# Kernel tuning notes

Hardware: AMD Instinct MI355X
Metric: run time of the kernel (lower is better)

The kernel has to match this reference:

```python
import jax, jax.numpy as jnp
import numpy as np

B, I, H, OH = 16384, 256, 256, 64
N_STEPS = 8  # fixed-step dopri5 (adaptive step control replaced by fixed grid for jit)


def setup_inputs() -> dict:
    key = jax.random.key(0)
    ks = jax.random.split(key, 12)
    sH = 1.0 / np.sqrt(H)
    sOH = 1.0 / np.sqrt(OH)
    u = lambda k, shape, s: jax.random.uniform(k, shape, jnp.float32, -s, s)
    return {
        "input": jax.random.normal(ks[0], (B, I), jnp.float32),
        "h_prev": jax.random.normal(ks[1], (B, H), jnp.float32),
        "c_prev": jax.random.normal(ks[2], (B, H), jnp.float32),
        "timespans": jax.random.uniform(ks[3], (B,), jnp.float32, 0.05, 1.0),
        # LSTMCell params (PyTorch layout: gates stacked as [i, f, g, o])
        "W_ih": u(ks[4], (4 * H, I), sH),
        "W_hh": u(ks[5], (4 * H, H), sH),
        "b_ih": u(ks[6], (4 * H,), sH),
        "b_hh": u(ks[7], (4 * H,), sH),
        # ode_func: Linear(H, OH) -> Tanh -> Linear(OH, H)
        "W1": u(ks[8], (OH, H), sH),
        "b1": u(ks[9], (OH,), sH),
        "W2": u(ks[10], (H, OH), sOH),
        "b2": u(ks[11], (H,), sOH),
    }


def reference(input, h_prev, c_prev, timespans, W_ih, W_hh, b_ih, b_hh, W1, b1, W2, b2):
    # --- LSTMCell ---
    gates = input @ W_ih.T + b_ih + h_prev @ W_hh.T + b_hh  # (B, 4H)
    gi, gf, gg, go = jnp.split(gates, 4, axis=-1)
    i = jax.nn.sigmoid(gi)
    f = jax.nn.sigmoid(gf)
    g = jnp.tanh(gg)
    o = jax.nn.sigmoid(go)
    c = f * c_prev + i * g
    h = o * jnp.tanh(c)

    # --- Neural ODE: dy/dt = MLP(y), autonomous, Dormand-Prince RK45 ---
    def ode_f(y):
        return jnp.tanh(y @ W1.T + b1) @ W2.T + b2

    dt = (timespans / N_STEPS)[:, None]  # (B, 1) per-sample step size

    def dopri5_step(y, _):
        k1 = ode_f(y)
        k2 = ode_f(y + dt * (1.0 / 5.0 * k1))
        k3 = ode_f(y + dt * (3.0 / 40.0 * k1 + 9.0 / 40.0 * k2))
        k4 = ode_f(y + dt * (44.0 / 45.0 * k1 - 56.0 / 15.0 * k2 + 32.0 / 9.0 * k3))
        k5 = ode_f(y + dt * (19372.0 / 6561.0 * k1 - 25360.0 / 2187.0 * k2
                             + 64448.0 / 6561.0 * k3 - 212.0 / 729.0 * k4))
        k6 = ode_f(y + dt * (9017.0 / 3168.0 * k1 - 355.0 / 33.0 * k2
                             + 46732.0 / 5247.0 * k3 + 49.0 / 176.0 * k4
                             - 5103.0 / 18656.0 * k5))
        y_next = y + dt * (35.0 / 384.0 * k1 + 500.0 / 1113.0 * k3 + 125.0 / 192.0 * k4
                           - 2187.0 / 6784.0 * k5 + 11.0 / 84.0 * k6)
        return y_next, None

    h_ode, _ = jax.lax.scan(dopri5_step, h, None, length=N_STEPS)
    return h_ode, c
```

## Files before the change

kernel.cpp:

```cpp
#include <hip/hip_runtime.h>
#include <hip/hip_bf16.h>


#define B_N 16384
#define H_N 256

typedef __attribute__((ext_vector_type(8))) short short8;
typedef __attribute__((ext_vector_type(4))) unsigned short u16x4;
typedef __attribute__((ext_vector_type(4))) float f32x4;

__device__ __forceinline__ unsigned short f2bf_s(float x) {
  __hip_bfloat16 h = __float2bfloat16(x);
  return *reinterpret_cast<unsigned short*>(&h);
}

__device__ __forceinline__ short8 pack8f(const float* p) {
  const f32x4 a = *(const f32x4*)p;
  const f32x4 b = *(const f32x4*)(p + 4);
  short8 r;
  r[0] = (short)f2bf_s(a[0]); r[1] = (short)f2bf_s(a[1]);
  r[2] = (short)f2bf_s(a[2]); r[3] = (short)f2bf_s(a[3]);
  r[4] = (short)f2bf_s(b[0]); r[5] = (short)f2bf_s(b[1]);
  r[6] = (short)f2bf_s(b[2]); r[7] = (short)f2bf_s(b[3]);
  return r;
}

__device__ __forceinline__ u16x4 pack4(f32x4 v) {
  u16x4 r;
  r[0] = f2bf_s(v[0]); r[1] = f2bf_s(v[1]);
  r[2] = f2bf_s(v[2]); r[3] = f2bf_s(v[3]);
  return r;
}

__device__ __forceinline__ float fast_sigmoid(float x) {
  return __builtin_amdgcn_rcpf(1.f + __expf(-x));
}
__device__ __forceinline__ float fast_tanh(float x) {
  x = fminf(15.f, fmaxf(-15.f, x));
  float e = __expf(2.f * x);
  return 1.f - 2.f * __builtin_amdgcn_rcpf(e + 1.f);
}

__device__ __forceinline__ void gl_lds16(const void* g, void* l) {
  __builtin_amdgcn_global_load_lds(
      (const __attribute__((address_space(1))) void*)g,
      (__attribute__((address_space(3))) void*)l, 16, 0, 0);
}

__global__ __launch_bounds__(256) void prep_kernel(
    const float* __restrict__ Wih, const float* __restrict__ Whh,
    const float* __restrict__ W1, const float* __restrict__ W2,
    const float* __restrict__ b2,
    unsigned short* __restrict__ wsB, unsigned short* __restrict__ wcB,
    float* __restrict__ uF) {
  const int bx = blockIdx.x;
  if (bx < 256) {
    int idx = bx * 256 + threadIdx.x;
    int n = idx >> 6, c = idx & 63, k = c * 8;
    const float* src = (k < 256) ? (Wih + (size_t)n * 256 + k)
                                 : (Whh + (size_t)n * 256 + (k - 256));
    *(short8*)(wsB + (size_t)n * 512 + k) = pack8f(src);
  } else if (bx < 272) {
    int idx = (bx - 256) * 256 + threadIdx.x;
    int f = idx >> 6, o = idx & 63;
    float a0 = 0.f, a1 = 0.f, a2 = 0.f, a3 = 0.f;
    for (int h = 0; h < 256; h += 4) {
      a0 = fmaf(W1[f * 256 + h],     W2[h * 64 + o],        a0);
      a1 = fmaf(W1[f * 256 + h + 1], W2[(h + 1) * 64 + o],  a1);
      a2 = fmaf(W1[f * 256 + h + 2], W2[(h + 2) * 64 + o],  a2);
      a3 = fmaf(W1[f * 256 + h + 3], W2[(h + 3) * 64 + o],  a3);
    }
    wcB[f * 64 + o] = f2bf_s((a0 + a1) + (a2 + a3));
  } else {
    int f = threadIdx.x;
    if (f < 64) {
      float a0 = 0.f, a1 = 0.f, a2 = 0.f, a3 = 0.f;
      for (int h = 0; h < 256; h += 4) {
        a0 = fmaf(W1[f * 256 + h],     b2[h],     a0);
        a1 = fmaf(W1[f * 256 + h + 1], b2[h + 1], a1);
        a2 = fmaf(W1[f * 256 + h + 2], b2[h + 2], a2);
        a3 = fmaf(W1[f * 256 + h + 3], b2[h + 3], a3);
      }
      uF[f] = (a0 + a1) + (a2 + a3);
    }
  }
}

__global__ __launch_bounds__(512, 4) void lstm_kernel(
    const float* __restrict__ x, const float* __restrict__ hp,
    const float* __restrict__ cp, const unsigned short* __restrict__ wsB,
    const float* __restrict__ bih, const float* __restrict__ bhh,
    float* __restrict__ out) {
  __shared__ __align__(16) float As2[2][128 * 32];
  __shared__ __align__(16) unsigned short Bs2[2][256 * 32];

  const int tid = threadIdx.x;
  const int lane = tid & 63;
  const int wv = tid >> 6;
  const int rg = wv >> 1;
  const int cg = wv & 1;
  const int s = lane & 15, q = lane >> 4;
  const int mb = blockIdx.x * 128;
  const int hb = blockIdx.y * 64;

  f32x4 acc[2][8];
#pragma unroll
  for (int mt = 0; mt < 2; ++mt)
#pragma unroll
    for (int tn = 0; tn < 8; ++tn) acc[mt][tn] = (f32x4){0.f, 0.f, 0.f, 0.f};

  const int c16a = wv * 2;
  const int rowA0 = c16a * 8 + (lane >> 3);
  const int gcA = (lane & 7) ^ (rowA0 & 7);
  const int rowB0 = c16a * 16 + (lane >> 2);
  const int rowB1 = rowB0 + 16;
  const int gcB0 = (lane & 3) ^ ((rowB0 >> 1) & 3);
  const int gcB1 = (lane & 3) ^ ((rowB1 >> 1) & 3);
  const int grB0 = (rowB0 >> 6) * 256 + hb + (rowB0 & 63);
  const int grB1 = (rowB1 >> 6) * 256 + hb + (rowB1 & 63);

  auto STAGE = [&](int buf, int kt) {
    const float* srcA = (kt < 8) ? x : hp;
    const int kl = (kt * 32) & 255;
    gl_lds16(srcA + (size_t)(mb + rowA0) * 256 + kl + gcA * 4,
             (char*)As2[buf] + c16a * 1024);
    gl_lds16(srcA + (size_t)(mb + rowA0 + 8) * 256 + kl + gcA * 4,
             (char*)As2[buf] + (c16a + 1) * 1024);
    gl_lds16(wsB + (size_t)grB0 * 512 + kt * 32 + gcB0 * 8,
             (char*)Bs2[buf] + c16a * 1024);
    gl_lds16(wsB + (size_t)grB1 * 512 + kt * 32 + gcB1 * 8,
             (char*)Bs2[buf] + (c16a + 1) * 1024);
  };

  STAGE(0, 0);
  __syncthreads();

  for (int kt = 0; kt < 16; ++kt) {
    const int buf = kt & 1;
    if (kt < 15) STAGE(buf ^ 1, kt + 1);

    short8 af[2];
#pragma unroll
    for (int mt = 0; mt < 2; ++mt) {
      const int ar = rg * 32 + mt * 16 + s;
      const char* ap = (const char*)As2[buf] + ar * 128;
      float tmp[8];
      *(f32x4*)tmp = *(const f32x4*)(ap + (((q * 2) ^ (ar & 7)) << 4));
      *(f32x4*)(tmp + 4) = *(const f32x4*)(ap + (((q * 2 + 1) ^ (ar & 7)) << 4));
      af[mt] = pack8f(tmp);
    }
    const char* bp = (const char*)Bs2[buf];
#pragma unroll
    for (int tn = 0; tn < 8; ++tn) {
      const int t = (tn >> 1) * 64 + cg * 32 + (tn & 1) * 16 + s;
      short8 bfr = *(const short8*)(bp + t * 64 + ((q ^ ((t >> 1) & 3)) << 4));
      acc[0][tn] = __builtin_amdgcn_mfma_f32_16x16x32_bf16(af[0], bfr, acc[0][tn], 0, 0, 0);
      acc[1][tn] = __builtin_amdgcn_mfma_f32_16x16x32_bf16(af[1], bfr, acc[1][tn], 0, 0, 0);
    }
    __syncthreads();
  }

#pragma unroll
  for (int mt = 0; mt < 2; ++mt)
#pragma unroll
    for (int ntl = 0; ntl < 2; ++ntl)
#pragma unroll
      for (int r = 0; r < 4; ++r) {
        int sample = mb + rg * 32 + mt * 16 + q * 4 + r;
        int h = hb + cg * 32 + ntl * 16 + s;
        float gi = acc[mt][0 + ntl][r] + bih[h] + bhh[h];
        float gf = acc[mt][2 + ntl][r] + bih[256 + h] + bhh[256 + h];
        float gg = acc[mt][4 + ntl][r] + bih[512 + h] + bhh[512 + h];
        float go = acc[mt][6 + ntl][r] + bih[768 + h] + bhh[768 + h];
        float iv = fast_sigmoid(gi), fv = fast_sigmoid(gf);
        float gv = fast_tanh(gg), ov = fast_sigmoid(go);
        float c = fv * cp[(size_t)sample * 256 + h] + iv * gv;
        float hv = ov * fast_tanh(c);
        out[(size_t)B_N * H_N + (size_t)sample * 256 + h] = c;
        out[(size_t)sample * 256 + h] = hv;
      }
}

__global__ __launch_bounds__(256, 4) void ode_kernel(
    float* __restrict__ out, const float* __restrict__ ts,
    const float* __restrict__ W1, const unsigned short* __restrict__ wcB,
    const float* __restrict__ uF, const float* __restrict__ W2,
    const float* __restrict__ b1, const float* __restrict__ b2) {
  __shared__ __align__(16) unsigned short zcA[16 * 64];
  __shared__ __align__(16) unsigned short zcB2[16 * 64];
  char* zA = (char*)zcA;
  char* zB = (char*)zcB2;

  const int tid = threadIdx.x;
  const int lane = tid & 63, wv = tid >> 6;
  const int s = lane & 15, q = lane >> 4;
  const int bb = blockIdx.x * 16;
  const int sx7 = s & 7;

  short8 wcf[2];
#pragma unroll
  for (int kt = 0; kt < 2; ++kt)
    wcf[kt] = *(const short8*)(wcB + (size_t)(wv * 16 + s) * 64 + kt * 32 + q * 8);

  const f32x4 b1v = *(const f32x4*)(b1 + wv * 16 + q * 4);
  const f32x4 u4 = *(const f32x4*)(uF + wv * 16 + q * 4);
  const float dt = ts[bb + s] * 0.125f;

  f32x4 yreg[4];
#pragma unroll
  for (int i = 0; i < 4; ++i)
    yreg[i] = *(const f32x4*)(out + (size_t)(bb + s) * 256 + wv * 64 + i * 16 + q * 4);

  f32x4 G = (f32x4){0.f, 0.f, 0.f, 0.f};
#pragma unroll
  for (int kt = 0; kt < 8; ++kt) {
    short8 w1f = pack8f(W1 + (size_t)(wv * 16 + s) * 256 + kt * 32 + q * 8);
    short8 yf = pack8f(out + (size_t)(bb + s) * 256 + kt * 32 + q * 8);
    G = __builtin_amdgcn_mfma_f32_16x16x32_bf16(w1f, yf, G, 0, 0, 0);
  }

  const int zwoff = (((wv * 2 + (q >> 1)) ^ sx7) << 4) + (q & 1) * 8;
  const int rb = s * 128;

  auto stz = [&](char* buf, f32x4 v) { *(u16x4*)(buf + rb + zwoff) = pack4(v); };
  auto wcmm = [&](const char* buf) -> f32x4 {
    const char* rp = buf + rb;
    short8 zf0 = *(const short8*)(rp + ((q ^ sx7) << 4));
    short8 zf1 = *(const short8*)(rp + (((4 + q) ^ sx7) << 4));
    f32x4 a = (f32x4){0.f, 0.f, 0.f, 0.f};
    a = __builtin_amdgcn_mfma_f32_16x16x32_bf16(wcf[0], zf0, a, 0, 0, 0);
    a = __builtin_amdgcn_mfma_f32_16x16x32_bf16(wcf[1], zf1, a, 0, 0, 0);
    return a;
  };
  auto stage = [&](char* buf, f32x4 zc, float cj) -> f32x4 {
    stz(buf, zc);
    __syncthreads();
    f32x4 o = wcmm(buf);
    f32x4 zo;
#pragma unroll
    for (int r = 0; r < 4; ++r)
      zo[r] = fast_tanh(fmaf(dt, fmaf(cj, u4[r], o[r]), G[r]) + b1v[r]);
    return zo;
  };

  const float A31 = 3.f / 40.f, A32 = 9.f / 40.f;
  const float A41 = 44.f / 45.f, A42 = -56.f / 15.f, A43 = 32.f / 9.f;
  const float A51 = 19372.f / 6561.f, A52 = -25360.f / 2187.f,
              A53 = 64448.f / 6561.f, A54 = -212.f / 729.f;
  const float A61 = 9017.f / 3168.f, A62 = -355.f / 33.f, A63 = 46732.f / 5247.f,
              A64 = 49.f / 176.f, A65 = -5103.f / 18656.f;
  const float C1 = 35.f / 384.f, C3 = 500.f / 1113.f, C4 = 125.f / 192.f,
              C5 = -2187.f / 6784.f, C6 = 11.f / 84.f;

  f32x4 SC = (f32x4){0.f, 0.f, 0.f, 0.f};

  for (int st = 0; st < 8; ++st) {
    f32x4 z1;
#pragma unroll
    for (int r = 0; r < 4; ++r) z1[r] = fast_tanh(G[r] + b1v[r]);

    f32x4 z2 = stage(zA, 0.2f * z1, 0.2f);
    f32x4 z3 = stage(zB, A31 * z1 + A32 * z2, 0.3f);
    f32x4 z4 = stage(zA, A41 * z1 + A42 * z2 + A43 * z3, 0.8f);
    f32x4 z5 = stage(zB, A51 * z1 + A52 * z2 + A53 * z3 + A54 * z4, 8.f / 9.f);
    f32x4 z6 = stage(zA, A61 * z1 + A62 * z2 + A63 * z3 + A64 * z4 + A65 * z5, 1.0f);

    f32x4 zc = C1 * z1 + C3 * z3 + C4 * z4 + C5 * z5 + C6 * z6;
    stz(zB, zc);
    __syncthreads();
    f32x4 o6 = wcmm(zB);
    SC += zc;
#pragma unroll
    for (int r = 0; r < 4; ++r) G[r] = fmaf(dt, u4[r] + o6[r], G[r]);
  }

  stz(zA, SC);
  __syncthreads();
  {
    const char* rp = zA + rb;
    short8 zf0 = *(const short8*)(rp + ((q ^ sx7) << 4));
    short8 zf1 = *(const short8*)(rp + (((4 + q) ^ sx7) << 4));
#pragma unroll
    for (int i = 0; i < 4; ++i) {
      short8 w2f0 = pack8f(W2 + (size_t)(wv * 64 + i * 16 + s) * 64 + q * 8);
      short8 w2f1 = pack8f(W2 + (size_t)(wv * 64 + i * 16 + s) * 64 + 32 + q * 8);
      f32x4 a = (f32x4){0.f, 0.f, 0.f, 0.f};
      a = __builtin_amdgcn_mfma_f32_16x16x32_bf16(w2f0, zf0, a, 0, 0, 0);
      a = __builtin_amdgcn_mfma_f32_16x16x32_bf16(w2f1, zf1, a, 0, 0, 0);
      f32x4 b2v = *(const f32x4*)(b2 + wv * 64 + i * 16 + q * 4);
#pragma unroll
      for (int r = 0; r < 4; ++r)
        yreg[i][r] = fmaf(dt, fmaf(8.f, b2v[r], a[r]), yreg[i][r]);
    }
  }

#pragma unroll
  for (int i = 0; i < 4; ++i)
    *(f32x4*)(out + (size_t)(bb + s) * 256 + wv * 64 + i * 16 + q * 4) = yreg[i];
}

extern "C" void kernel_launch(void* const* d_in, const int* in_sizes, int n_in,
                              void* d_out, int out_size, void* d_ws, size_t ws_size,
                              hipStream_t stream) {
  const float* x   = (const float*)d_in[0];
  const float* hp  = (const float*)d_in[1];
  const float* cp  = (const float*)d_in[2];
  const float* ts  = (const float*)d_in[3];
  const float* Wih = (const float*)d_in[4];
  const float* Whh = (const float*)d_in[5];
  const float* bih = (const float*)d_in[6];
  const float* bhh = (const float*)d_in[7];
  const float* W1  = (const float*)d_in[8];
  const float* b1  = (const float*)d_in[9];
  const float* W2  = (const float*)d_in[10];
  const float* b2  = (const float*)d_in[11];
  float* out = (float*)d_out;

  unsigned short* wsB = (unsigned short*)d_ws;
  unsigned short* wcB = wsB + 1024 * 512;
  float* uF = (float*)((char*)d_ws + 1024 * 1024 + 8192);

  prep_kernel<<<273, 256, 0, stream>>>(Wih, Whh, W1, W2, b2, wsB, wcB, uF);
  lstm_kernel<<<dim3(128, 4), 512, 0, stream>>>(x, hp, cp, wsB, bih, bhh, out);
  ode_kernel<<<1024, 256, 0, stream>>>(out, ts, W1, wcB, uF, W2, b1, b2);
}
```

Measured before the change: 79.05 us.

## Run ODE solver with one wave per block to drop block barriers

Restructures the ODE kernel from four waves per 16-sample block to a single 64-lane wave. That wave computes all four 16-column tiles of the hidden projection, so the per-stage z exchange through LDS needs only a waitcnt instead of __syncthreads. W1 and W2 are pre-converted to bf16 in the prep kernel rather than packed per block. The tanh clamp is also removed. The single-wave blocks carry more registers per lane and give less latency hiding per block. Without the clamp, exp overflow to inf in tanh still gives ±1 through rcp, so it should stay safe.

```diff
diff --git a/kernel.cpp b/kernel.cpp
--- a/kernel.cpp
+++ b/kernel.cpp
@@ -36,7 +36,6 @@
   return __builtin_amdgcn_rcpf(1.f + __expf(-x));
 }
 __device__ __forceinline__ float fast_tanh(float x) {
-  x = fminf(15.f, fmaxf(-15.f, x));
   float e = __expf(2.f * x);
   return 1.f - 2.f * __builtin_amdgcn_rcpf(e + 1.f);
 }
@@ -52,7 +51,8 @@
     const float* __restrict__ W1, const float* __restrict__ W2,
     const float* __restrict__ b2,
     unsigned short* __restrict__ wsB, unsigned short* __restrict__ wcB,
-    float* __restrict__ uF) {
+    float* __restrict__ uF, unsigned short* __restrict__ w1B,
+    unsigned short* __restrict__ w2B) {
   const int bx = blockIdx.x;
   if (bx < 256) {
     int idx = bx * 256 + threadIdx.x;
@@ -71,7 +71,7 @@
       a3 = fmaf(W1[f * 256 + h + 3], W2[(h + 3) * 64 + o],  a3);
     }
     wcB[f * 64 + o] = f2bf_s((a0 + a1) + (a2 + a3));
-  } else {
+  } else if (bx == 272) {
     int f = threadIdx.x;
     if (f < 64) {
       float a0 = 0.f, a1 = 0.f, a2 = 0.f, a3 = 0.f;
@@ -83,6 +83,12 @@
       }
       uF[f] = (a0 + a1) + (a2 + a3);
     }
+  } else if (bx < 281) {
+    int idx = (bx - 273) * 256 + threadIdx.x;
+    *(short8*)(w1B + (size_t)idx * 8) = pack8f(W1 + (size_t)idx * 8);
+  } else {
+    int idx = (bx - 281) * 256 + threadIdx.x;
+    *(short8*)(w2B + (size_t)idx * 8) = pack8f(W2 + (size_t)idx * 8);
   }
 }
 
@@ -181,66 +187,74 @@
       }
 }
 
-__global__ __launch_bounds__(256, 4) void ode_kernel(
+__global__ __launch_bounds__(64) void ode_kernel(
     float* __restrict__ out, const float* __restrict__ ts,
-    const float* __restrict__ W1, const unsigned short* __restrict__ wcB,
-    const float* __restrict__ uF, const float* __restrict__ W2,
+    const unsigned short* __restrict__ wcB, const float* __restrict__ uF,
+    const unsigned short* __restrict__ w1B, const unsigned short* __restrict__ w2B,
     const float* __restrict__ b1, const float* __restrict__ b2) {
-  __shared__ __align__(16) unsigned short zcA[16 * 64];
-  __shared__ __align__(16) unsigned short zcB2[16 * 64];
-  char* zA = (char*)zcA;
-  char* zB = (char*)zcB2;
-
-  const int tid = threadIdx.x;
-  const int lane = tid & 63, wv = tid >> 6;
+  __shared__ __align__(16) unsigned short zbuf[16 * 80];
+  char* zb = (char*)zbuf;
+
+  const int lane = threadIdx.x;
   const int s = lane & 15, q = lane >> 4;
   const int bb = blockIdx.x * 16;
-  const int sx7 = s & 7;
-
-  short8 wcf[2];
-#pragma unroll
-  for (int kt = 0; kt < 2; ++kt)
-    wcf[kt] = *(const short8*)(wcB + (size_t)(wv * 16 + s) * 64 + kt * 32 + q * 8);
-
-  const f32x4 b1v = *(const f32x4*)(b1 + wv * 16 + q * 4);
-  const f32x4 u4 = *(const f32x4*)(uF + wv * 16 + q * 4);
+  const int wb = s * 160;
+
+  short8 wcf[4][2];
+#pragma unroll
+  for (int i = 0; i < 4; ++i)
+#pragma unroll
+    for (int kt = 0; kt < 2; ++kt)
+      wcf[i][kt] = *(const short8*)(wcB + (size_t)(i * 16 + s) * 64 + kt * 32 + q * 8);
+  f32x4 b1v[4], u4[4];
+#pragma unroll
+  for (int i = 0; i < 4; ++i) {
+    b1v[i] = *(const f32x4*)(b1 + i * 16 + q * 4);
+    u4[i] = *(const f32x4*)(uF + i * 16 + q * 4);
+  }
   const float dt = ts[bb + s] * 0.125f;
 
-  f32x4 yreg[4];
-#pragma unroll
-  for (int i = 0; i < 4; ++i)
-    yreg[i] = *(const f32x4*)(out + (size_t)(bb + s) * 256 + wv * 64 + i * 16 + q * 4);
-
-  f32x4 G = (f32x4){0.f, 0.f, 0.f, 0.f};
+  f32x4 G[4];
+#pragma unroll
+  for (int i = 0; i < 4; ++i) G[i] = (f32x4){0.f, 0.f, 0.f, 0.f};
 #pragma unroll
   for (int kt = 0; kt < 8; ++kt) {
-    short8 w1f = pack8f(W1 + (size_t)(wv * 16 + s) * 256 + kt * 32 + q * 8);
     short8 yf = pack8f(out + (size_t)(bb + s) * 256 + kt * 32 + q * 8);
-    G = __builtin_amdgcn_mfma_f32_16x16x32_bf16(w1f, yf, G, 0, 0, 0);
-  }
-
-  const int zwoff = (((wv * 2 + (q >> 1)) ^ sx7) << 4) + (q & 1) * 8;
-  const int rb = s * 128;
-
-  auto stz = [&](char* buf, f32x4 v) { *(u16x4*)(buf + rb + zwoff) = pack4(v); };
-  auto wcmm = [&](const char* buf) -> f32x4 {
-    const char* rp = buf + rb;
-    short8 zf0 = *(const short8*)(rp + ((q ^ sx7) << 4));
-    short8 zf1 = *(const short8*)(rp + (((4 + q) ^ sx7) << 4));
-    f32x4 a = (f32x4){0.f, 0.f, 0.f, 0.f};
-    a = __builtin_amdgcn_mfma_f32_16x16x32_bf16(wcf[0], zf0, a, 0, 0, 0);
-    a = __builtin_amdgcn_mfma_f32_16x16x32_bf16(wcf[1], zf1, a, 0, 0, 0);
-    return a;
+#pragma unroll
+    for (int i = 0; i < 4; ++i) {
+      short8 w1f = *(const short8*)(w1B + (size_t)(i * 16 + s) * 256 + kt * 32 + q * 8);
+      G[i] = __builtin_amdgcn_mfma_f32_16x16x32_bf16(w1f, yf, G[i], 0, 0, 0);
+    }
+  }
+
+  auto exch = [&](const f32x4 (&v)[4]) {
+#pragma unroll
+    for (int i = 0; i < 4; ++i)
+      *(u16x4*)(zb + wb + i * 32 + q * 8) = pack4(v[i]);
+    asm volatile("s_waitcnt lgkmcnt(0)" ::: "memory");
+    __builtin_amdgcn_sched_barrier(0);
   };
-  auto stage = [&](char* buf, f32x4 zc, float cj) -> f32x4 {
-    stz(buf, zc);
-    __syncthreads();
-    f32x4 o = wcmm(buf);
-    f32x4 zo;
-#pragma unroll
-    for (int r = 0; r < 4; ++r)
-      zo[r] = fast_tanh(fmaf(dt, fmaf(cj, u4[r], o[r]), G[r]) + b1v[r]);
-    return zo;
+  auto wcmm = [&](f32x4 (&o)[4]) {
+    short8 zf0 = *(const short8*)(zb + wb + q * 16);
+    short8 zf1 = *(const short8*)(zb + wb + 64 + q * 16);
+#pragma unroll
+    for (int i = 0; i < 4; ++i) {
+      f32x4 a = (f32x4){0.f, 0.f, 0.f, 0.f};
+      a = __builtin_amdgcn_mfma_f32_16x16x32_bf16(wcf[i][0], zf0, a, 0, 0, 0);
+      a = __builtin_amdgcn_mfma_f32_16x16x32_bf16(wcf[i][1], zf1, a, 0, 0, 0);
+      o[i] = a;
+    }
+  };
+  auto stage = [&](const f32x4 (&zc)[4], float cj, f32x4 (&zo)[4]) {
+    exch(zc);
+    f32x4 o[4];
+    wcmm(o);
+#pragma unroll
+    for (int i = 0; i < 4; ++i)
+#pragma unroll
+      for (int r = 0; r < 4; ++r)
+        zo[i][r] =
+            fast_tanh(fmaf(dt, fmaf(cj, u4[i][r], o[i][r]), G[i][r]) + b1v[i][r]);
   };
 
   const float A31 = 3.f / 40.f, A32 = 9.f / 40.f;
@@ -252,51 +266,80 @@
   const float C1 = 35.f / 384.f, C3 = 500.f / 1113.f, C4 = 125.f / 192.f,
               C5 = -2187.f / 6784.f, C6 = 11.f / 84.f;
 
-  f32x4 SC = (f32x4){0.f, 0.f, 0.f, 0.f};
+  f32x4 SC[4];
+#pragma unroll
+  for (int i = 0; i < 4; ++i) SC[i] = (f32x4){0.f, 0.f, 0.f, 0.f};
+  f32x4 z1[4], z2[4], z3[4], z4[4], z5[4], zc[4];
 
   for (int st = 0; st < 8; ++st) {
-    f32x4 z1;
-#pragma unroll
-    for (int r = 0; r < 4; ++r) z1[r] = fast_tanh(G[r] + b1v[r]);
-
-    f32x4 z2 = stage(zA, 0.2f * z1, 0.2f);
-    f32x4 z3 = stage(zB, A31 * z1 + A32 * z2, 0.3f);
-    f32x4 z4 = stage(zA, A41 * z1 + A42 * z2 + A43 * z3, 0.8f);
-    f32x4 z5 = stage(zB, A51 * z1 + A52 * z2 + A53 * z3 + A54 * z4, 8.f / 9.f);
-    f32x4 z6 = stage(zA, A61 * z1 + A62 * z2 + A63 * z3 + A64 * z4 + A65 * z5, 1.0f);
-
-    f32x4 zc = C1 * z1 + C3 * z3 + C4 * z4 + C5 * z5 + C6 * z6;
-    stz(zB, zc);
-    __syncthreads();
-    f32x4 o6 = wcmm(zB);
-    SC += zc;
-#pragma unroll
-    for (int r = 0; r < 4; ++r) G[r] = fmaf(dt, u4[r] + o6[r], G[r]);
-  }
-
-  stz(zA, SC);
-  __syncthreads();
+#pragma unroll
+    for (int i = 0; i < 4; ++i)
+#pragma unroll
+      for (int r = 0; r < 4; ++r) z1[i][r] = fast_tanh(G[i][r] + b1v[i][r]);
+
+#pragma unroll
+    for (int i = 0; i < 4; ++i) zc[i] = 0.2f * z1[i];
+    stage(zc, 0.2f, z2);
+#pragma unroll
+    for (int i = 0; i < 4; ++i) zc[i] = A31 * z1[i] + A32 * z2[i];
+    stage(zc, 0.3f, z3);
+#pragma unroll
+    for (int i = 0; i < 4; ++i) zc[i] = A41 * z1[i] + A42 * z2[i] + A43 * z3[i];
+    stage(zc, 0.8f, z4);
+#pragma unroll
+    for (int i = 0; i < 4; ++i)
+      zc[i] = A51 * z1[i] + A52 * z2[i] + A53 * z3[i] + A54 * z4[i];
+    stage(zc, 8.f / 9.f, z5);
+#pragma unroll
+    for (int i = 0; i < 4; ++i)
+      zc[i] = A61 * z1[i] + A62 * z2[i] + A63 * z3[i] + A64 * z4[i] + A65 * z5[i];
+    exch(zc);
+    {
+      f32x4 o[4];
+      wcmm(o);
+#pragma unroll
+      for (int i = 0; i < 4; ++i)
+#pragma unroll
+        for (int r = 0; r < 4; ++r) {
+          float z6v =
+              fast_tanh(fmaf(dt, fmaf(1.0f, u4[i][r], o[i][r]), G[i][r]) + b1v[i][r]);
+          zc[i][r] = C1 * z1[i][r] + C3 * z3[i][r] + C4 * z4[i][r] +
+                     C5 * z5[i][r] + C6 * z6v;
+        }
+    }
+    exch(zc);
+    {
+      f32x4 o6[4];
+      wcmm(o6);
+#pragma unroll
+      for (int i = 0; i < 4; ++i) {
+        SC[i] += zc[i];
+#pragma unroll
+        for (int r = 0; r < 4; ++r)
+          G[i][r] = fmaf(dt, u4[i][r] + o6[i][r], G[i][r]);
+      }
+    }
+  }
+
+  exch(SC);
   {
-    const char* rp = zA + rb;
-    short8 zf0 = *(const short8*)(rp + ((q ^ sx7) << 4));
-    short8 zf1 = *(const short8*)(rp + (((4 + q) ^ sx7) << 4));
-#pragma unroll
-    for (int i = 0; i < 4; ++i) {
-      short8 w2f0 = pack8f(W2 + (size_t)(wv * 64 + i * 16 + s) * 64 + q * 8);
-      short8 w2f1 = pack8f(W2 + (size_t)(wv * 64 + i * 16 + s) * 64 + 32 + q * 8);
+    short8 zf0 = *(const short8*)(zb + wb + q * 16);
+    short8 zf1 = *(const short8*)(zb + wb + 64 + q * 16);
+#pragma unroll
+    for (int ft = 0; ft < 16; ++ft) {
+      short8 w2a = *(const short8*)(w2B + (size_t)(ft * 16 + s) * 64 + q * 8);
+      short8 w2b = *(const short8*)(w2B + (size_t)(ft * 16 + s) * 64 + 32 + q * 8);
       f32x4 a = (f32x4){0.f, 0.f, 0.f, 0.f};
-      a = __builtin_amdgcn_mfma_f32_16x16x32_bf16(w2f0, zf0, a, 0, 0, 0);
-      a = __builtin_amdgcn_mfma_f32_16x16x32_bf16(w2f1, zf1, a, 0, 0, 0);
-      f32x4 b2v = *(const f32x4*)(b2 + wv * 64 + i * 16 + q * 4);
+      a = __builtin_amdgcn_mfma_f32_16x16x32_bf16(w2a, zf0, a, 0, 0, 0);
+      a = __builtin_amdgcn_mfma_f32_16x16x32_bf16(w2b, zf1, a, 0, 0, 0);
+      f32x4 y0 = *(const f32x4*)(out + (size_t)(bb + s) * 256 + ft * 16 + q * 4);
+      f32x4 b2v = *(const f32x4*)(b2 + ft * 16 + q * 4);
 #pragma unroll
       for (int r = 0; r < 4; ++r)
-        yreg[i][r] = fmaf(dt, fmaf(8.f, b2v[r], a[r]), yreg[i][r]);
-    }
-  }
-
-#pragma unroll
-  for (int i = 0; i < 4; ++i)
-    *(f32x4*)(out + (size_t)(bb + s) * 256 + wv * 64 + i * 16 + q * 4) = yreg[i];
+        y0[r] = fmaf(dt, fmaf(8.f, b2v[r], a[r]), y0[r]);
+      *(f32x4*)(out + (size_t)(bb + s) * 256 + ft * 16 + q * 4) = y0;
+    }
+  }
 }
 
 extern "C" void kernel_launch(void* const* d_in, const int* in_sizes, int n_in,
@@ -317,10 +360,12 @@
   float* out = (float*)d_out;
 
   unsigned short* wsB = (unsigned short*)d_ws;
-  unsigned short* wcB = wsB + 1024 * 512;
-  float* uF = (float*)((char*)d_ws + 1024 * 1024 + 8192);
-
-  prep_kernel<<<273, 256, 0, stream>>>(Wih, Whh, W1, W2, b2, wsB, wcB, uF);
+  unsigned short* wcB = (unsigned short*)((char*)d_ws + 1048576);
+  float* uF = (float*)((char*)d_ws + 1048576 + 8192);
+  unsigned short* w1B = (unsigned short*)((char*)d_ws + 1048576 + 16384);
+  unsigned short* w2B = (unsigned short*)((char*)d_ws + 1048576 + 49152);
+
+  prep_kernel<<<289, 256, 0, stream>>>(Wih, Whh, W1, W2, b2, wsB, wcB, uF, w1B, w2B);
   lstm_kernel<<<dim3(128, 4), 512, 0, stream>>>(x, hp, cp, wsB, bih, bhh, out);
-  ode_kernel<<<1024, 256, 0, stream>>>(out, ts, W1, wcB, uF, W2, b1, b2);
-}
+  ode_kernel<<<1024, 64, 0, stream>>>(out, ts, wcB, uF, w1B, w2B, b1, b2);
+}
```

Result: slower. 84.11 us (+6.4%).
